# Kernel optimization log

Hardware: AMD Instinct MI355X
Metric: run time of the kernel (lower is better)

## Reference

```python
import jax, jax.numpy as jnp
from jax import lax
import numpy as np

B, C, H, W = 4, 128, 96, 96
K = 3            # kernel_size (taps)
KS = 4           # scope size (weight_shape)
PAD = 1
G = 1            # rotation_groups


def setup_inputs() -> dict:
    key = jax.random.key(0)
    k1, k2, k3, k4 = jax.random.split(key, 4)
    x = jax.random.normal(k1, (B, C, H, W), jnp.float32)
    rot_w = jax.random.normal(k2, (G * K * K * 2, C, K, K), jnp.float32) * 0.01  # zero-init-ish
    rot_b = jax.random.normal(k3, (G * K * K * 2,), jnp.float32) * 0.01
    weight = jax.random.normal(k4, (C, KS, KS), jnp.float32) * 0.1  # depthwise scope weights
    return {"x": x, "rot_w": rot_w, "rot_b": rot_b, "weight": weight}


def _fc_bias():
    # base tap coordinates inside the KSxKS scope (weight_dilate = 1)
    start = (KS - (K - 1) - 1) / 2.0  # 0.5
    vals = []
    for i in range(K):
        for j in range(K):
            vals += [start + i, start + j]
    return jnp.asarray(np.tile(np.array(vals, np.float32), G))  # (G*K*K*2,)


def reference(x, rot_w, rot_b, weight):
    # --- rotation conv: predicts per-location (h,w) offsets per tap ---
    rot = lax.conv_general_dilated(
        x, rot_w, window_strides=(1, 1), padding=[(PAD, PAD), (PAD, PAD)],
        dimension_numbers=("NCHW", "OIHW", "NCHW"))
    rot = rot + rot_b[None, :, None, None]  # (B, G*K*K*2, H, W)

    # --- 'scope' clipping: absolute coord = rot + base, clamped to scope ---
    fcb = _fc_bias()
    coord = jnp.clip(rot + fcb[None, :, None, None], 0.0, KS - 1)
    coord = coord.reshape(B, K * K, 2, H, W)  # G == 1
    ch, cw = coord[:, :, 0], coord[:, :, 1]    # (B, 9, H, W)

    # --- bilinear sampling of the per-channel scope weight ---
    h0 = jnp.floor(ch); w0 = jnp.floor(cw)
    lh = ch - h0; lw = cw - w0
    h0i = jnp.clip(h0.astype(jnp.int32), 0, KS - 1)
    w0i = jnp.clip(w0.astype(jnp.int32), 0, KS - 1)
    h1i = jnp.clip(h0i + 1, 0, KS - 1)
    w1i = jnp.clip(w0i + 1, 0, KS - 1)
    wflat = weight.reshape(C, KS * KS)

    def gather(hi, wi):
        return wflat[:, hi * KS + wi]  # (C, B, 9, H, W)

    w_samp = (gather(h0i, w0i) * ((1 - lh) * (1 - lw))[None]
              + gather(h0i, w1i) * ((1 - lh) * lw)[None]
              + gather(h1i, w0i) * (lh * (1 - lw))[None]
              + gather(h1i, w1i) * (lh * lw)[None])
    w_samp = jnp.transpose(w_samp, (1, 0, 2, 3, 4))  # (B, C, 9, H, W)

    # --- depthwise conv with per-location sampled weights ---
    xp = jnp.pad(x, ((0, 0), (0, 0), (PAD, PAD), (PAD, PAD)))
    patches = jnp.stack([xp[:, :, i:i + H, j:j + W]
                         for i in range(K) for j in range(K)], axis=2)  # (B, C, 9, H, W)
    return jnp.sum(w_samp * patches, axis=2)  # (B, C, H, W)
```

## Files before the change

kernel.cpp:

```cpp
#include <hip/hip_runtime.h>
#include <hip/hip_fp16.h>

#define Bdim 4
#define Cdim 128
#define Hdim 96
#define Wdim 96
#define HW   (Hdim*Wdim)
#define NOC  18

typedef __attribute__((ext_vector_type(8))) short bf16x8;
typedef __attribute__((ext_vector_type(4))) float f32x4;
typedef _Float16 h2 __attribute__((ext_vector_type(2)));

__device__ inline short f2bf(float f) {
    unsigned u = __float_as_uint(f);
    unsigned r = (u + 0x7FFFu + ((u >> 16) & 1u)) >> 16;
    return (short)r;
}

__device__ inline unsigned pkh2(float a, float b) {
    return (unsigned)__half_as_ushort(__float2half(a)) |
           ((unsigned)__half_as_ushort(__float2half(b)) << 16);
}

__global__ __launch_bounds__(256) void prep_kernel(const float* __restrict__ x,
                                                   const float* __restrict__ rot_w,
                                                   const float* __restrict__ weight,
                                                   short* __restrict__ xnh,
                                                   short* __restrict__ wpk,
                                                   uint4* __restrict__ wtab) {
    __shared__ short ldsT[96 * 72];
    const int bid = blockIdx.x;
    const int t   = threadIdx.x;

    if (bid < 768) {
        int b = bid / 192;
        int h = (bid / 2) % 96;
        int c0 = (bid & 1) * 64;
        const float* xs = x + ((size_t)(b * Cdim + c0) * Hdim + h) * Wdim;
#pragma unroll
        for (int i = 0; i < 24; ++i) {
            int idx = i * 256 + t;
            int w  = idx % 96;
            int ci = idx / 96;
            ldsT[w * 72 + ci] = f2bf(xs[(size_t)ci * HW + w]);
        }
        __syncthreads();
        short* dst = xnh + (((size_t)b * 98 + (h + 1)) * 98 + 1) * 128 + c0;
#pragma unroll
        for (int j = 0; j < 3; ++j) {
            int idx = j * 256 + t;
            int c8 = idx % 8;
            int w  = idx / 8;
            *(bf16x8*)(dst + (size_t)w * 128 + c8 * 8) = *(const bf16x8*)&ldsT[w * 72 + c8 * 8];
        }
    } else if (bid < 776) {
        int z = bid - 768;
        int b = z / 2;
        int r = (z & 1) ? 97 : 0;
        short* base = xnh + ((size_t)b * 98 + r) * 98 * 128;
        bf16x8 zero = {0,0,0,0,0,0,0,0};
        for (int i = t; i < 1568; i += 256)
            ((bf16x8*)base)[i] = zero;
    } else if (bid < 784) {
        int z = bid - 776;
        int b = z / 2;
        int col = (z & 1) ? 97 : 0;
        bf16x8 zero = {0,0,0,0,0,0,0,0};
        for (int i = t; i < 1536; i += 256) {
            int r  = 1 + i / 16;
            int c8 = i % 16;
            *(bf16x8*)(xnh + (((size_t)b * 98 + r) * 98 + col) * 128 + c8 * 8) = zero;
        }
    } else if (bid < 928) {
        int f = (bid - 784) * 256 + t;
        int e    = f & 7;
        int l    = (f >> 3) & 63;
        int ch   = (f >> 9) & 3;
        int tap  = (f >> 11) % 9;
        int mt   = f / 18432;
        int oc = mt * 16 + (l & 15);
        int c  = ch * 32 + (l >> 4) * 8 + e;
        float v = (oc < NOC) ? rot_w[(size_t)oc * (Cdim * 9) + c * 9 + tap] : 0.f;
        wpk[f] = f2bf(v);
    } else {
        for (int i = t; i < 576; i += 256) {
            int e = i >> 6;
            int l = i & 63;
            int r = e / 3, s = e % 3;
            const float* w0p = weight + (size_t)(2 * l) * 16;
            uint4 v;
            v.x = pkh2(w0p[r * 4 + s],      w0p[r * 4 + s + 1]);
            v.y = pkh2(w0p[r * 4 + s + 4],  w0p[r * 4 + s + 5]);
            v.z = pkh2(w0p[16 + r * 4 + s],     w0p[16 + r * 4 + s + 1]);
            v.w = pkh2(w0p[16 + r * 4 + s + 4], w0p[16 + r * 4 + s + 5]);
            wtab[i] = v;
        }
    }
}

__global__ __launch_bounds__(256) void fused_kernel(const short* __restrict__ xnh,
                                                    const short* __restrict__ wpk,
                                                    const float* __restrict__ rot_b,
                                                    const uint4* __restrict__ wtab,
                                                    float* __restrict__ out) {
    __shared__ uint4 wq4[9][64];
    __shared__ float dsc[4 * 16 * 20];
    __shared__ uint2 cq2[144];
    __shared__ uint4 lidq[16];
    __shared__ float ot[16][130];

    const int tid  = threadIdx.x;
    const int lane = tid & 63;
    const int wv   = tid >> 6;

    for (int i = tid; i < 576; i += 256)
        ((uint4*)wq4)[i] = wtab[i];

    const int tile = blockIdx.x;
    const int b    = tile / 576;
    const int hw0  = (tile % 576) * 16;
    const int h    = hw0 / Wdim;
    const int w0   = hw0 % Wdim;

    {
        const int px = lane & 15, kg = lane >> 4;
        f32x4 acc0 = {0,0,0,0};
        f32x4 acc1 = {0,0,0,0};
        const short* xb = xnh + (((size_t)b * 98 + h) * 98 + (w0 + px)) * 128
                          + wv * 32 + kg * 8;
        const short* wA = wpk + (size_t)wv * 512 + lane * 8;

        bf16x8 Bc  = *(const bf16x8*)(xb);
        bf16x8 A0c = *(const bf16x8*)(wA);
        bf16x8 A1c = *(const bf16x8*)(wA + 9 * 4 * 512);
#pragma unroll
        for (int tap = 0; tap < 9; ++tap) {
            bf16x8 Bn, A0n, A1n;
            if (tap < 8) {
                const int di = (tap + 1) / 3, dj = (tap + 1) % 3;
                Bn  = *(const bf16x8*)(xb + (di * 98 + dj) * 128);
                A0n = *(const bf16x8*)(wA + (size_t)(tap + 1) * 4 * 512);
                A1n = *(const bf16x8*)(wA + (size_t)(9 + tap + 1) * 4 * 512);
            }
            acc0 = __builtin_amdgcn_mfma_f32_16x16x32_bf16(A0c, Bc, acc0, 0, 0, 0);
            acc1 = __builtin_amdgcn_mfma_f32_16x16x32_bf16(A1c, Bc, acc1, 0, 0, 0);
            if (tap < 8) { Bc = Bn; A0c = A0n; A1c = A1n; }
        }
        float* ds = dsc + ((wv * 16) + px) * 20;
        *(f32x4*)(ds + kg * 4) = acc0;
        if (kg == 0) { ds[16] = acc1[0]; ds[17] = acc1[1]; }
    }
    __syncthreads();

    if (tid < 144) {
        const int px = tid / 9;
        const int t9 = tid - px * 9;
        const int i = t9 / 3, j = t9 % 3;
        float ch = rot_b[2 * t9]     + (0.5f + (float)i);
        float cw = rot_b[2 * t9 + 1] + (0.5f + (float)j);
#pragma unroll
        for (int k = 0; k < 4; ++k) {
            const float* ds = dsc + ((k * 16) + px) * 20;
            ch += ds[2 * t9];
            cw += ds[2 * t9 + 1];
        }
        ch = fminf(fmaxf(ch, 0.f), 3.f);
        cw = fminf(fmaxf(cw, 0.f), 3.f);
        float h0f = floorf(ch), w0f = floorf(cw);
        float lh = ch - h0f, lw = cw - w0f;
        int h0 = (int)h0f, w0i = (int)w0f;
        float bh0 = 1.f - lh;
        float aw0 = 1.f - lw;
        if (h0 >= 3)  { h0 = 2;  bh0 = 0.f; }
        if (w0i >= 3) { w0i = 2; aw0 = 0.f; }
        float q00 = aw0 * bh0;
        float q01 = (1.f - aw0) * bh0;
        float q10 = aw0 * (1.f - bh0);
        float q11 = (1.f - aw0) * (1.f - bh0);
        uint2 cf;
        cf.x = pkh2(q00, q01);
        cf.y = pkh2(q10, q11);
        cq2[px * 9 + t9] = cf;
        ((unsigned char*)lidq)[px * 16 + t9] = (unsigned char)(h0 * 3 + w0i);
    }
    __syncthreads();

    const unsigned* xbase =
        (const unsigned*)(xnh + (((size_t)b * 98 + h) * 98 + (w0 + 4 * wv)) * 128) + lane;
    unsigned xw[3][6];
#pragma unroll
    for (int r = 0; r < 3; ++r)
#pragma unroll
        for (int j = 0; j < 6; ++j)
            xw[r][j] = xbase[(r * 98 + j) * 64];

    float acc0[4], acc1[4];
#pragma unroll
    for (int p = 0; p < 4; ++p) { acc0[p] = 0.f; acc1[p] = 0.f; }

#pragma unroll
    for (int pp = 0; pp < 4; ++pp) {
        const int p = 4 * wv + pp;
        uint4 lw = lidq[p];
        uint4 g[9];
        uint2 cf[9];
#pragma unroll
        for (int t = 0; t < 9; ++t) {
            unsigned idx = (((const unsigned*)&lw)[t >> 2] >> (8 * (t & 3))) & 0xFu;
            g[t]  = wq4[idx][lane];
            cf[t] = cq2[p * 9 + t];
        }
#pragma unroll
        for (int t = 0; t < 9; ++t) {
            unsigned xu = xw[t / 3][pp + (t % 3)];
            float x0 = __uint_as_float(xu << 16);
            float x1 = __uint_as_float(xu & 0xFFFF0000u);
            float s0 = __builtin_amdgcn_fdot2(__builtin_bit_cast(h2, cf[t].x),
                                              __builtin_bit_cast(h2, g[t].x), 0.f, false);
            s0 = __builtin_amdgcn_fdot2(__builtin_bit_cast(h2, cf[t].y),
                                        __builtin_bit_cast(h2, g[t].y), s0, false);
            float s1 = __builtin_amdgcn_fdot2(__builtin_bit_cast(h2, cf[t].x),
                                              __builtin_bit_cast(h2, g[t].z), 0.f, false);
            s1 = __builtin_amdgcn_fdot2(__builtin_bit_cast(h2, cf[t].y),
                                        __builtin_bit_cast(h2, g[t].w), s1, false);
            acc0[pp] = fmaf(s0, x0, acc0[pp]);
            acc1[pp] = fmaf(s1, x1, acc1[pp]);
        }
    }

#pragma unroll
    for (int pp = 0; pp < 4; ++pp)
        *(float2*)&ot[4 * wv + pp][2 * lane] = make_float2(acc0[pp], acc1[pp]);
    __syncthreads();

    const int px = tid & 15;
    const int cr = tid >> 4;
    float* ob = out + (size_t)b * Cdim * HW + hw0 + px;
#pragma unroll
    for (int k = 0; k < 8; ++k) {
        int ci = cr * 8 + k;
        ob[(size_t)ci * HW] = ot[px][ci];
    }
}

extern "C" void kernel_launch(void* const* d_in, const int* in_sizes, int n_in,
                              void* d_out, int out_size, void* d_ws, size_t ws_size,
                              hipStream_t stream) {
    const float* x      = (const float*)d_in[0];
    const float* rot_w  = (const float*)d_in[1];
    const float* rot_b  = (const float*)d_in[2];
    const float* weight = (const float*)d_in[3];
    float* out = (float*)d_out;

    char* ws = (char*)d_ws;
    const size_t xnh_bytes = (size_t)Bdim * 98 * 98 * 128 * 2;
    const size_t wpk_bytes = (size_t)2 * 9 * 4 * 64 * 8 * 2;

    short* xnh  = (short*)ws;
    short* wpk  = (short*)(ws + xnh_bytes);
    uint4* wtab = (uint4*)(ws + xnh_bytes + wpk_bytes);

    prep_kernel<<<929, 256, 0, stream>>>(x, rot_w, weight, xnh, wpk, wtab);
    fused_kernel<<<2304, 256, 0, stream>>>(xnh, wpk, rot_b, wtab, out);
}
```

Before: 36.52 us.

## Restructure fused kernel to single-wave blocks with wave barriers and direct stores

Each block now has one 64-lane wave instead of four. That wave does the full 128-channel offset-prediction MFMA reduction itself, using split accumulators, so the cross-wave LDS reduction is gone. The block-wide __syncthreads are replaced with wave barriers, and the LDS transpose buffer for output is dropped in favour of direct float4 stores per channel. This removes block synchronisation and LDS traffic, but each block now does four times the serial work with less latency hiding per block and more scattered global stores.

Measured after the change: 45.95 us. +25.8%, slower.

```diff
diff --git a/kernel.cpp b/kernel.cpp
--- a/kernel.cpp
+++ b/kernel.cpp
@@ -99,148 +99,145 @@
     }
 }
 
-__global__ __launch_bounds__(256) void fused_kernel(const short* __restrict__ xnh,
-                                                    const short* __restrict__ wpk,
-                                                    const float* __restrict__ rot_b,
-                                                    const uint4* __restrict__ wtab,
-                                                    float* __restrict__ out) {
+__global__ __launch_bounds__(64) void fused_kernel(const short* __restrict__ xnh,
+                                                   const short* __restrict__ wpk,
+                                                   const float* __restrict__ rot_b,
+                                                   const uint4* __restrict__ wtab,
+                                                   float* __restrict__ out) {
     __shared__ uint4 wq4[9][64];
-    __shared__ float dsc[4 * 16 * 20];
+    __shared__ float dsc[16 * 20];
     __shared__ uint2 cq2[144];
     __shared__ uint4 lidq[16];
-    __shared__ float ot[16][130];
-
-    const int tid  = threadIdx.x;
-    const int lane = tid & 63;
-    const int wv   = tid >> 6;
-
-    for (int i = tid; i < 576; i += 256)
-        ((uint4*)wq4)[i] = wtab[i];
+
+    const int lane = threadIdx.x;
+
+#pragma unroll
+    for (int i = 0; i < 9; ++i)
+        ((uint4*)wq4)[i * 64 + lane] = wtab[i * 64 + lane];
 
     const int tile = blockIdx.x;
     const int b    = tile / 576;
     const int hw0  = (tile % 576) * 16;
     const int h    = hw0 / Wdim;
     const int w0   = hw0 % Wdim;
+    const int px   = lane & 15, kg = lane >> 4;
+
+    f32x4 a00 = {0,0,0,0}, a01 = {0,0,0,0};
+    f32x4 a10 = {0,0,0,0}, a11 = {0,0,0,0};
+    const short* xb = xnh + (((size_t)b * 98 + h) * 98 + (w0 + px)) * 128 + kg * 8;
+    const short* wA = wpk + lane * 8;
+#pragma unroll
+    for (int tap = 0; tap < 9; ++tap) {
+        const int di = tap / 3, dj = tap % 3;
+        const short* xr = xb + (di * 98 + dj) * 128;
+#pragma unroll
+        for (int ch = 0; ch < 4; ++ch) {
+            bf16x8 B  = *(const bf16x8*)(xr + ch * 32);
+            bf16x8 A0 = *(const bf16x8*)(wA + (size_t)(tap * 4 + ch) * 512);
+            bf16x8 A1 = *(const bf16x8*)(wA + (size_t)((9 + tap) * 4 + ch) * 512);
+            if (ch & 1) {
+                a01 = __builtin_amdgcn_mfma_f32_16x16x32_bf16(A0, B, a01, 0, 0, 0);
+                a11 = __builtin_amdgcn_mfma_f32_16x16x32_bf16(A1, B, a11, 0, 0, 0);
+            } else {
+                a00 = __builtin_amdgcn_mfma_f32_16x16x32_bf16(A0, B, a00, 0, 0, 0);
+                a10 = __builtin_amdgcn_mfma_f32_16x16x32_bf16(A1, B, a10, 0, 0, 0);
+            }
+        }
+    }
+    f32x4 acc0 = a00 + a01;
+    f32x4 acc1 = a10 + a11;
 
     {
-        const int px = lane & 15, kg = lane >> 4;
-        f32x4 acc0 = {0,0,0,0};
-        f32x4 acc1 = {0,0,0,0};
-        const short* xb = xnh + (((size_t)b * 98 + h) * 98 + (w0 + px)) * 128
-                          + wv * 32 + kg * 8;
-        const short* wA = wpk + (size_t)wv * 512 + lane * 8;
-
-        bf16x8 Bc  = *(const bf16x8*)(xb);
-        bf16x8 A0c = *(const bf16x8*)(wA);
-        bf16x8 A1c = *(const bf16x8*)(wA + 9 * 4 * 512);
-#pragma unroll
-        for (int tap = 0; tap < 9; ++tap) {
-            bf16x8 Bn, A0n, A1n;
-            if (tap < 8) {
-                const int di = (tap + 1) / 3, dj = (tap + 1) % 3;
-                Bn  = *(const bf16x8*)(xb + (di * 98 + dj) * 128);
-                A0n = *(const bf16x8*)(wA + (size_t)(tap + 1) * 4 * 512);
-                A1n = *(const bf16x8*)(wA + (size_t)(9 + tap + 1) * 4 * 512);
-            }
-            acc0 = __builtin_amdgcn_mfma_f32_16x16x32_bf16(A0c, Bc, acc0, 0, 0, 0);
-            acc1 = __builtin_amdgcn_mfma_f32_16x16x32_bf16(A1c, Bc, acc1, 0, 0, 0);
-            if (tap < 8) { Bc = Bn; A0c = A0n; A1c = A1n; }
-        }
-        float* ds = dsc + ((wv * 16) + px) * 20;
+        float* ds = dsc + px * 20;
         *(f32x4*)(ds + kg * 4) = acc0;
         if (kg == 0) { ds[16] = acc1[0]; ds[17] = acc1[1]; }
     }
-    __syncthreads();
-
-    if (tid < 144) {
-        const int px = tid / 9;
-        const int t9 = tid - px * 9;
-        const int i = t9 / 3, j = t9 % 3;
-        float ch = rot_b[2 * t9]     + (0.5f + (float)i);
-        float cw = rot_b[2 * t9 + 1] + (0.5f + (float)j);
-#pragma unroll
-        for (int k = 0; k < 4; ++k) {
-            const float* ds = dsc + ((k * 16) + px) * 20;
-            ch += ds[2 * t9];
-            cw += ds[2 * t9 + 1];
-        }
-        ch = fminf(fmaxf(ch, 0.f), 3.f);
-        cw = fminf(fmaxf(cw, 0.f), 3.f);
-        float h0f = floorf(ch), w0f = floorf(cw);
-        float lh = ch - h0f, lw = cw - w0f;
-        int h0 = (int)h0f, w0i = (int)w0f;
-        float bh0 = 1.f - lh;
-        float aw0 = 1.f - lw;
-        if (h0 >= 3)  { h0 = 2;  bh0 = 0.f; }
-        if (w0i >= 3) { w0i = 2; aw0 = 0.f; }
-        float q00 = aw0 * bh0;
-        float q01 = (1.f - aw0) * bh0;
-        float q10 = aw0 * (1.f - bh0);
-        float q11 = (1.f - aw0) * (1.f - bh0);
-        uint2 cf;
-        cf.x = pkh2(q00, q01);
-        cf.y = pkh2(q10, q11);
-        cq2[px * 9 + t9] = cf;
-        ((unsigned char*)lidq)[px * 16 + t9] = (unsigned char)(h0 * 3 + w0i);
-    }
-    __syncthreads();
-
-    const unsigned* xbase =
-        (const unsigned*)(xnh + (((size_t)b * 98 + h) * 98 + (w0 + 4 * wv)) * 128) + lane;
-    unsigned xw[3][6];
-#pragma unroll
-    for (int r = 0; r < 3; ++r)
-#pragma unroll
-        for (int j = 0; j < 6; ++j)
-            xw[r][j] = xbase[(r * 98 + j) * 64];
-
-    float acc0[4], acc1[4];
-#pragma unroll
-    for (int p = 0; p < 4; ++p) { acc0[p] = 0.f; acc1[p] = 0.f; }
-
-#pragma unroll
-    for (int pp = 0; pp < 4; ++pp) {
-        const int p = 4 * wv + pp;
-        uint4 lw = lidq[p];
-        uint4 g[9];
-        uint2 cf[9];
-#pragma unroll
-        for (int t = 0; t < 9; ++t) {
-            unsigned idx = (((const unsigned*)&lw)[t >> 2] >> (8 * (t & 3))) & 0xFu;
-            g[t]  = wq4[idx][lane];
-            cf[t] = cq2[p * 9 + t];
-        }
-#pragma unroll
-        for (int t = 0; t < 9; ++t) {
-            unsigned xu = xw[t / 3][pp + (t % 3)];
-            float x0 = __uint_as_float(xu << 16);
-            float x1 = __uint_as_float(xu & 0xFFFF0000u);
-            float s0 = __builtin_amdgcn_fdot2(__builtin_bit_cast(h2, cf[t].x),
-                                              __builtin_bit_cast(h2, g[t].x), 0.f, false);
-            s0 = __builtin_amdgcn_fdot2(__builtin_bit_cast(h2, cf[t].y),
-                                        __builtin_bit_cast(h2, g[t].y), s0, false);
-            float s1 = __builtin_amdgcn_fdot2(__builtin_bit_cast(h2, cf[t].x),
-                                              __builtin_bit_cast(h2, g[t].z), 0.f, false);
-            s1 = __builtin_amdgcn_fdot2(__builtin_bit_cast(h2, cf[t].y),
-                                        __builtin_bit_cast(h2, g[t].w), s1, false);
-            acc0[pp] = fmaf(s0, x0, acc0[pp]);
-            acc1[pp] = fmaf(s1, x1, acc1[pp]);
-        }
-    }
-
-#pragma unroll
-    for (int pp = 0; pp < 4; ++pp)
-        *(float2*)&ot[4 * wv + pp][2 * lane] = make_float2(acc0[pp], acc1[pp]);
-    __syncthreads();
-
-    const int px = tid & 15;
-    const int cr = tid >> 4;
-    float* ob = out + (size_t)b * Cdim * HW + hw0 + px;
-#pragma unroll
-    for (int k = 0; k < 8; ++k) {
-        int ci = cr * 8 + k;
-        ob[(size_t)ci * HW] = ot[px][ci];
+    __builtin_amdgcn_wave_barrier();
+
+    {
+        const int px2 = lane & 15, tq = lane >> 4;
+        if (tq < 3) {
+            const float* dr = dsc + px2 * 20;
+#pragma unroll
+            for (int k = 0; k < 3; ++k) {
+                int t9 = tq * 3 + k;
+                int i = t9 / 3, j = t9 % 3;
+                float ch = dr[2 * t9]     + rot_b[2 * t9]     + (0.5f + (float)i);
+                float cw = dr[2 * t9 + 1] + rot_b[2 * t9 + 1] + (0.5f + (float)j);
+                ch = fminf(fmaxf(ch, 0.f), 3.f);
+                cw = fminf(fmaxf(cw, 0.f), 3.f);
+                float h0f = floorf(ch), w0f = floorf(cw);
+                float lh = ch - h0f, lw = cw - w0f;
+                int h0 = (int)h0f, w0i = (int)w0f;
+                float bh0 = 1.f - lh;
+                float aw0 = 1.f - lw;
+                if (h0 >= 3)  { h0 = 2;  bh0 = 0.f; }
+                if (w0i >= 3) { w0i = 2; aw0 = 0.f; }
+                float q00 = aw0 * bh0;
+                float q01 = (1.f - aw0) * bh0;
+                float q10 = aw0 * (1.f - bh0);
+                float q11 = (1.f - aw0) * (1.f - bh0);
+                uint2 cf;
+                cf.x = pkh2(q00, q01);
+                cf.y = pkh2(q10, q11);
+                cq2[px2 * 9 + t9] = cf;
+                ((unsigned char*)lidq)[px2 * 16 + t9] = (unsigned char)(h0 * 3 + w0i);
+            }
+        }
+    }
+    __builtin_amdgcn_wave_barrier();
+
+#pragma unroll
+    for (int sub = 0; sub < 4; ++sub) {
+        const int pbase = sub * 4;
+        const unsigned* xbase =
+            (const unsigned*)(xnh + (((size_t)b * 98 + h) * 98 + (w0 + pbase)) * 128) + lane;
+        unsigned xw[3][6];
+#pragma unroll
+        for (int r = 0; r < 3; ++r)
+#pragma unroll
+            for (int j = 0; j < 6; ++j)
+                xw[r][j] = xbase[(r * 98 + j) * 64];
+
+        float o0[4], o1[4];
+#pragma unroll
+        for (int p = 0; p < 4; ++p) { o0[p] = 0.f; o1[p] = 0.f; }
+
+#pragma unroll
+        for (int pp = 0; pp < 4; ++pp) {
+            const int p = pbase + pp;
+            uint4 lw = lidq[p];
+            uint4 g[9];
+            uint2 cf[9];
+#pragma unroll
+            for (int t = 0; t < 9; ++t) {
+                unsigned idx = (((const unsigned*)&lw)[t >> 2] >> (8 * (t & 3))) & 0xFu;
+                g[t]  = wq4[idx][lane];
+                cf[t] = cq2[p * 9 + t];
+            }
+#pragma unroll
+            for (int t = 0; t < 9; ++t) {
+                unsigned xu = xw[t / 3][pp + (t % 3)];
+                float x0 = __uint_as_float(xu << 16);
+                float x1 = __uint_as_float(xu & 0xFFFF0000u);
+                float s0 = __builtin_amdgcn_fdot2(__builtin_bit_cast(h2, cf[t].x),
+                                                  __builtin_bit_cast(h2, g[t].x), 0.f, false);
+                s0 = __builtin_amdgcn_fdot2(__builtin_bit_cast(h2, cf[t].y),
+                                            __builtin_bit_cast(h2, g[t].y), s0, false);
+                float s1 = __builtin_amdgcn_fdot2(__builtin_bit_cast(h2, cf[t].x),
+                                                  __builtin_bit_cast(h2, g[t].z), 0.f, false);
+                s1 = __builtin_amdgcn_fdot2(__builtin_bit_cast(h2, cf[t].y),
+                                            __builtin_bit_cast(h2, g[t].w), s1, false);
+                o0[pp] = fmaf(s0, x0, o0[pp]);
+                o1[pp] = fmaf(s1, x1, o1[pp]);
+            }
+        }
+
+        float4 v0 = make_float4(o0[0], o0[1], o0[2], o0[3]);
+        float4 v1 = make_float4(o1[0], o1[1], o1[2], o1[3]);
+        float* ob = out + ((size_t)b * Cdim + 2 * lane) * HW + hw0 + pbase;
+        *(float4*)ob = v0;
+        *(float4*)(ob + HW) = v1;
     }
 }
 
@@ -262,5 +259,5 @@
     uint4* wtab = (uint4*)(ws + xnh_bytes + wpk_bytes);
 
     prep_kernel<<<929, 256, 0, stream>>>(x, rot_w, weight, xnh, wpk, wtab);
-    fused_kernel<<<2304, 256, 0, stream>>>(xnh, wpk, rot_b, wtab, out);
-}
+    fused_kernel<<<2304, 64, 0, stream>>>(xnh, wpk, rot_b, wtab, out);
+}
```
